# Kernel optimization log

Hardware: AMD Instinct MI355X
Metric: run time of the kernel (lower is better)

## Reference

```python
import jax, jax.numpy as jnp
import numpy as np

B, S, D_IN, D_OUT = 4, 2048, 4096, 4096
NNZ = 167772


def setup_inputs() -> dict:
    key = jax.random.key(0)
    k_x, k_w, k_b, k_v, k_r, k_c = jax.random.split(key, 6)
    x = jax.random.normal(k_x, (B, S, D_IN), dtype=jnp.float32)
    W = jax.random.normal(k_w, (D_OUT, D_IN), dtype=jnp.float32) * 0.02
    b = jax.random.normal(k_b, (D_OUT,), dtype=jnp.float32) * 0.01
    delta_vals = jax.random.normal(k_v, (NNZ,), dtype=jnp.float32) * 0.01
    delta_rows = jax.random.randint(k_r, (NNZ,), 0, D_OUT)
    delta_cols = jax.random.randint(k_c, (NNZ,), 0, D_IN)
    return {"x": x, "W": W, "b": b, "delta_vals": delta_vals,
            "delta_rows": delta_rows, "delta_cols": delta_cols}


def reference(x, W, b, delta_vals, delta_rows, delta_cols):
    # output_sparse = pruned nn.Linear(x)
    out_sparse = jnp.einsum('bsi,oi->bso', x, W) + b
    # delta_B_csr as dense [out, in] built by scatter-add (duplicate coords sum, like CSR assembly)
    delta = jnp.zeros((D_OUT, D_IN), dtype=jnp.float32).at[delta_rows, delta_cols].add(delta_vals)
    # torch.sparse.mm(delta, x2d.T).T == x2d @ delta.T, computed in fp32
    comp = jnp.einsum('bsi,oi->bso', x.astype(jnp.float32), delta).astype(x.dtype)
    return out_sparse + comp
```

## Files before the change

kernel.cpp:

```cpp
#include <hip/hip_runtime.h>
#include <hip/hip_bf16.h>
#include <stdint.h>

#define B_    4
#define S_    2048
#define DIN   4096
#define DOUT  4096
#define NNZ_  167772
#define M_    (B_*S_)

typedef __attribute__((ext_vector_type(4))) float f32x4;
typedef __attribute__((ext_vector_type(8))) short s16x8;
typedef __attribute__((ext_vector_type(8))) unsigned short u16x8;

__device__ __forceinline__ unsigned short f2bf(float f) {
    unsigned int u = __float_as_uint(f);
    u += 0x7FFFu + ((u >> 16) & 1u);
    return (unsigned short)(u >> 16);
}

__device__ __forceinline__ float bf2f(unsigned short h) {
    return __uint_as_float(((unsigned int)h) << 16);
}

__device__ __forceinline__ void gload16(const void* g, void* l) {
    __builtin_amdgcn_global_load_lds(
        (const __attribute__((address_space(1))) unsigned int*)g,
        (__attribute__((address_space(3))) unsigned int*)l,
        16, 0, 0);
}


__global__ void cvt_both_kernel(const float* __restrict__ W,
                                const float* __restrict__ x,
                                unsigned short* __restrict__ Wb,
                                unsigned short* __restrict__ xb,
                                int n8w, int n8x) {
    int i = blockIdx.x * blockDim.x + threadIdx.x;
    const float* src;
    unsigned short* dst;
    int j;
    if (i < n8w) { src = W; dst = Wb; j = i; }
    else         { src = x; dst = xb; j = i - n8w; if (j >= n8x) return; }
    const f32x4* s4 = reinterpret_cast<const f32x4*>(src);
    f32x4 a0 = s4[2*j], a1 = s4[2*j+1];
    u16x8 o;
    o[0]=f2bf(a0[0]); o[1]=f2bf(a0[1]); o[2]=f2bf(a0[2]); o[3]=f2bf(a0[3]);
    o[4]=f2bf(a1[0]); o[5]=f2bf(a1[1]); o[6]=f2bf(a1[2]); o[7]=f2bf(a1[3]);
    reinterpret_cast<u16x8*>(dst)[j] = o;
}

__global__ void scatter_bf16_kernel(const float* __restrict__ vals,
                                    const int* __restrict__ rows,
                                    const int* __restrict__ cols,
                                    unsigned short* __restrict__ Wb, int nnz) {
    int i = blockIdx.x * blockDim.x + threadIdx.x;
    if (i >= nnz) return;
    size_t cell = (size_t)rows[i] * DIN + cols[i];
    unsigned int* word = reinterpret_cast<unsigned int*>(Wb) + (cell >> 1);
    const bool hiHalf = (cell & 1) != 0;
    const float v = vals[i];
    unsigned int old = *word, assumed;
    do {
        assumed = old;
        unsigned short h = hiHalf ? (unsigned short)(assumed >> 16)
                                  : (unsigned short)(assumed & 0xFFFFu);
        unsigned short nh = f2bf(bf2f(h) + v);
        unsigned int nw = hiHalf ? ((assumed & 0x0000FFFFu) | ((unsigned int)nh << 16))
                                 : ((assumed & 0xFFFF0000u) | (unsigned int)nh);
        old = atomicCAS(word, assumed, nw);
    } while (old != assumed);
}


__global__ __launch_bounds__(512, 2) void gemm_kernel(
    const unsigned short* __restrict__ A,
    const unsigned short* __restrict__ Bw,
    const float* __restrict__ bias,
    float* __restrict__ C)
{
    constexpr int K  = DIN;
    constexpr int N  = DOUT;
    constexpr int KB = K * 2;
    extern __shared__ char smem[];

    const int tid  = threadIdx.x;
    const int wave = tid >> 6;
    const int lane = tid & 63;
    const int wr = wave >> 2;
    const int wc = wave & 3;
    const int l16 = lane & 15;
    const int kq  = lane >> 4;
    const int s7  = l16 & 7;

    const int wg  = blockIdx.x;
    const int swz = (wg & 7) * 64 + (wg >> 3);
    const int bx  = swz & 15;
    const int by  = swz >> 4;
    const int rowBase = by * 256;
    const int colBase = bx * 256;

    const int r0    = tid >> 3;
    const int gslot = (tid & 7) ^ (r0 & 7);
    const char* gA = (const char*)A  + (size_t)(rowBase + r0) * KB + gslot * 16;
    const char* gB = (const char*)Bw + (size_t)(colBase + r0) * KB + gslot * 16;
    const int wvoff = wave * 1024;

    const unsigned q0 = (unsigned)(kq ^ s7);
    const unsigned q1 = (unsigned)((4 + kq) ^ s7);
    const unsigned aBase = (unsigned)((wr * 128 + l16) * 128);
    const unsigned bBase = (unsigned)((wc * 64  + l16) * 128);
    const unsigned short* aPtr[2][2];
    const unsigned short* bPtr[2][2];
    #pragma unroll
    for (int p_ = 0; p_ < 2; ++p_) {
        aPtr[p_][0] = (const unsigned short*)(smem + p_ * 65536 + aBase + q0 * 16);
        aPtr[p_][1] = (const unsigned short*)(smem + p_ * 65536 + aBase + q1 * 16);
        bPtr[p_][0] = (const unsigned short*)(smem + p_ * 65536 + 32768 + bBase + q0 * 16);
        bPtr[p_][1] = (const unsigned short*)(smem + p_ * 65536 + 32768 + bBase + q1 * 16);
    }

    f32x4 acc[8][4];
    #pragma unroll
    for (int i = 0; i < 8; ++i)
        #pragma unroll
        for (int j = 0; j < 4; ++j) acc[i][j] = f32x4{0.f, 0.f, 0.f, 0.f};

#define STAGE_A(P, T, H) do { \
    const char* g_ = gA + (size_t)(T) * 128 + (size_t)(H) * 1048576; \
    gload16(g_,          smem + (P) * 65536 + (H) * 16384 + wvoff); \
    gload16(g_ + 524288, smem + (P) * 65536 + (H) * 16384 + 8192 + wvoff); \
} while (0)

#define STAGE_B(P, T, H) do { \
    const char* g_ = gB + (size_t)(T) * 128 + (size_t)(H) * 1048576; \
    gload16(g_,          smem + (P) * 65536 + 32768 + (H) * 16384 + wvoff); \
    gload16(g_ + 524288, smem + (P) * 65536 + 32768 + (H) * 16384 + 8192 + wvoff); \
} while (0)

#define BAR() asm volatile("s_barrier" ::: "memory")

#define TILE(P, T, SB, SA, VN) do { \
    s16x8 af0[4][2], af1[4][2], bf0[2][2], bf1[2][2]; \
     \
    _Pragma("unroll") \
    for (int m_ = 0; m_ < 4; ++m_) { \
        af0[m_][0] = *(const s16x8*)(aPtr[P][0] + m_ * 1024); \
        af0[m_][1] = *(const s16x8*)(aPtr[P][1] + m_ * 1024); } \
    _Pragma("unroll") \
    for (int n_ = 0; n_ < 2; ++n_) { \
        bf0[n_][0] = *(const s16x8*)(bPtr[P][0] + n_ * 1024); \
        bf0[n_][1] = *(const s16x8*)(bPtr[P][1] + n_ * 1024); } \
    if (SB) STAGE_B(1 - (P), (T) + 1, 0); \
    BAR(); \
    __builtin_amdgcn_s_setprio(1); \
    _Pragma("unroll") \
    for (int m_ = 0; m_ < 4; ++m_) \
      _Pragma("unroll") \
      for (int n_ = 0; n_ < 2; ++n_) { \
        acc[m_][n_] = __builtin_amdgcn_mfma_f32_16x16x32_bf16(af0[m_][0], bf0[n_][0], acc[m_][n_], 0, 0, 0); \
        acc[m_][n_] = __builtin_amdgcn_mfma_f32_16x16x32_bf16(af0[m_][1], bf0[n_][1], acc[m_][n_], 0, 0, 0); } \
    __builtin_amdgcn_s_setprio(0); \
    BAR(); \
     \
    _Pragma("unroll") \
    for (int m_ = 0; m_ < 4; ++m_) { \
        af1[m_][0] = *(const s16x8*)(aPtr[P][0] + 4096 + m_ * 1024); \
        af1[m_][1] = *(const s16x8*)(aPtr[P][1] + 4096 + m_ * 1024); } \
    if (SB) STAGE_B(1 - (P), (T) + 1, 1); \
    BAR(); \
    __builtin_amdgcn_s_setprio(1); \
    _Pragma("unroll") \
    for (int m_ = 0; m_ < 4; ++m_) \
      _Pragma("unroll") \
      for (int n_ = 0; n_ < 2; ++n_) { \
        acc[4 + m_][n_] = __builtin_amdgcn_mfma_f32_16x16x32_bf16(af1[m_][0], bf0[n_][0], acc[4 + m_][n_], 0, 0, 0); \
        acc[4 + m_][n_] = __builtin_amdgcn_mfma_f32_16x16x32_bf16(af1[m_][1], bf0[n_][1], acc[4 + m_][n_], 0, 0, 0); } \
    __builtin_amdgcn_s_setprio(0); \
    BAR(); \
     \
    _Pragma("unroll") \
    for (int n_ = 0; n_ < 2; ++n_) { \
        bf1[n_][0] = *(const s16x8*)(bPtr[P][0] + 2048 + n_ * 1024); \
        bf1[n_][1] = *(const s16x8*)(bPtr[P][1] + 2048 + n_ * 1024); } \
    if (SA) STAGE_A(P, (T) + 2, 0); \
    BAR(); \
    __builtin_amdgcn_s_setprio(1); \
    _Pragma("unroll") \
    for (int m_ = 0; m_ < 4; ++m_) \
      _Pragma("unroll") \
      for (int n_ = 0; n_ < 2; ++n_) { \
        acc[m_][2 + n_] = __builtin_amdgcn_mfma_f32_16x16x32_bf16(af0[m_][0], bf1[n_][0], acc[m_][2 + n_], 0, 0, 0); \
        acc[m_][2 + n_] = __builtin_amdgcn_mfma_f32_16x16x32_bf16(af0[m_][1], bf1[n_][1], acc[m_][2 + n_], 0, 0, 0); } \
    __builtin_amdgcn_s_setprio(0); \
    BAR(); \
     \
    if (SA) STAGE_A(P, (T) + 2, 1); \
    BAR(); \
    __builtin_amdgcn_s_setprio(1); \
    _Pragma("unroll") \
    for (int m_ = 0; m_ < 4; ++m_) \
      _Pragma("unroll") \
      for (int n_ = 0; n_ < 2; ++n_) { \
        acc[4 + m_][2 + n_] = __builtin_amdgcn_mfma_f32_16x16x32_bf16(af1[m_][0], bf1[n_][0], acc[4 + m_][2 + n_], 0, 0, 0); \
        acc[4 + m_][2 + n_] = __builtin_amdgcn_mfma_f32_16x16x32_bf16(af1[m_][1], bf1[n_][1], acc[4 + m_][2 + n_], 0, 0, 0); } \
    __builtin_amdgcn_s_setprio(0); \
     \
    if (VN) { asm volatile("s_waitcnt vmcnt(4)" ::: "memory"); } \
    else    { asm volatile("s_waitcnt vmcnt(0)" ::: "memory"); } \
    BAR(); \
} while (0)

    STAGE_A(0, 0, 0); STAGE_A(0, 0, 1);
    STAGE_B(0, 0, 0); STAGE_B(0, 0, 1);
    STAGE_A(1, 1, 0); STAGE_A(1, 1, 1);
    asm volatile("s_waitcnt vmcnt(4)" ::: "memory");
    BAR();

    #pragma unroll 1
    for (int t = 0; t < 62; t += 2) {
        TILE(0, t,     1, 1, 4);
        TILE(1, t + 1, 1, 1, 4);
    }
    TILE(0, 62, 1, 0, 0);
    TILE(1, 63, 0, 0, 0);

#undef TILE
#undef BAR
#undef STAGE_A
#undef STAGE_B

    float bv[4];
    #pragma unroll
    for (int nf = 0; nf < 4; ++nf)
        bv[nf] = bias[colBase + wc * 64 + nf * 16 + l16];

    #pragma unroll
    for (int mf = 0; mf < 8; ++mf) {
        const int rowG = rowBase + wr * 128 + mf * 16 + kq * 4;
        float* cp = C + (size_t)rowG * N + colBase + wc * 64 + l16;
        #pragma unroll
        for (int nf = 0; nf < 4; ++nf)
            #pragma unroll
            for (int j = 0; j < 4; ++j)
                cp[(size_t)j * N + nf * 16] = acc[mf][nf][j] + bv[nf];
    }
}

extern "C" void kernel_launch(void* const* d_in, const int* in_sizes, int n_in,
                              void* d_out, int out_size, void* d_ws, size_t ws_size,
                              hipStream_t stream) {
    const float* x     = (const float*)d_in[0];
    const float* W     = (const float*)d_in[1];
    const float* b     = (const float*)d_in[2];
    const float* dvals = (const float*)d_in[3];
    const int*   drows = (const int*)d_in[4];
    const int*   dcols = (const int*)d_in[5];
    float* out = (float*)d_out;

    char* ws = (char*)d_ws;
    unsigned short* Wb = (unsigned short*)ws;
    unsigned short* xb = (unsigned short*)(ws + (size_t)32 * 1024 * 1024);

    int n8w = DOUT * DIN / 8;
    int n8x = M_ * DIN / 8;
    int nblk = (n8w + n8x) / 256;
    cvt_both_kernel<<<nblk, 256, 0, stream>>>(W, x, Wb, xb, n8w, n8x);
    scatter_bf16_kernel<<<(NNZ_ + 255) / 256, 256, 0, stream>>>(dvals, drows, dcols, Wb, NNZ_);

    static bool attr_done = false;
    if (!attr_done) {
        (void)hipFuncSetAttribute(reinterpret_cast<const void*>(gemm_kernel),
                                  hipFuncAttributeMaxDynamicSharedMemorySize, 131072);
        attr_done = true;
    }
    gemm_kernel<<<dim3(512), dim3(512), 131072, stream>>>(xb, Wb, b, out);
}
```

Measured before the change: 275.6 us.

## Restructure GEMM tile pipeline to prefetch next-tile fragments and stage both operands ahead

Reorders the four MFMA quadrants in each K-tile so the first A/B fragments for the next tile are read from LDS during the current tile's last quadrants. Global-to-LDS staging of A and B for tile T+2 is moved to the end of the tile, so both operands are now double-buffered two tiles ahead. This replaces the old split where B led by one tile and A by two. The aim is to hide LDS read latency and simplify the vmcnt waits, at the cost of more live registers for fragments carried across iterations. The stricter vmcnt(0) waits and changed barrier placement could expose global-load latency or create LDS buffer hazards.

```diff
diff --git a/kernel.cpp b/kernel.cpp
--- a/kernel.cpp
+++ b/kernel.cpp
@@ -126,6 +126,8 @@
         #pragma unroll
         for (int j = 0; j < 4; ++j) acc[i][j] = f32x4{0.f, 0.f, 0.f, 0.f};
 
+    s16x8 af0[4][2], af1[4][2], bf0[2][2], bf1[2][2];
+
 #define STAGE_A(P, T, H) do { \
     const char* g_ = gA + (size_t)(T) * 128 + (size_t)(H) * 1048576; \
     gload16(g_,          smem + (P) * 65536 + (H) * 16384 + wvoff); \
@@ -140,92 +142,99 @@
 
 #define BAR() asm volatile("s_barrier" ::: "memory")
 
-#define TILE(P, T, SB, SA, VN) do { \
-    s16x8 af0[4][2], af1[4][2], bf0[2][2], bf1[2][2]; \
-     \
-    _Pragma("unroll") \
-    for (int m_ = 0; m_ < 4; ++m_) { \
-        af0[m_][0] = *(const s16x8*)(aPtr[P][0] + m_ * 1024); \
-        af0[m_][1] = *(const s16x8*)(aPtr[P][1] + m_ * 1024); } \
+#define MFMA16(D, Af, Bf) D = __builtin_amdgcn_mfma_f32_16x16x32_bf16(Af, Bf, D, 0, 0, 0)
+
+#define TILE(P, T, SS, FN) do { \
+     \
+    BAR(); \
+    __builtin_amdgcn_s_setprio(1); \
+    _Pragma("unroll") \
+    for (int m_ = 0; m_ < 4; ++m_) \
+      _Pragma("unroll") \
+      for (int n_ = 0; n_ < 2; ++n_) { \
+        MFMA16(acc[m_][n_], af0[m_][0], bf0[n_][0]); \
+        MFMA16(acc[m_][n_], af0[m_][1], bf0[n_][1]); } \
+    __builtin_amdgcn_s_setprio(0); \
     _Pragma("unroll") \
     for (int n_ = 0; n_ < 2; ++n_) { \
-        bf0[n_][0] = *(const s16x8*)(bPtr[P][0] + n_ * 1024); \
-        bf0[n_][1] = *(const s16x8*)(bPtr[P][1] + n_ * 1024); } \
-    if (SB) STAGE_B(1 - (P), (T) + 1, 0); \
-    BAR(); \
-    __builtin_amdgcn_s_setprio(1); \
-    _Pragma("unroll") \
-    for (int m_ = 0; m_ < 4; ++m_) \
-      _Pragma("unroll") \
-      for (int n_ = 0; n_ < 2; ++n_) { \
-        acc[m_][n_] = __builtin_amdgcn_mfma_f32_16x16x32_bf16(af0[m_][0], bf0[n_][0], acc[m_][n_], 0, 0, 0); \
-        acc[m_][n_] = __builtin_amdgcn_mfma_f32_16x16x32_bf16(af0[m_][1], bf0[n_][1], acc[m_][n_], 0, 0, 0); } \
-    __builtin_amdgcn_s_setprio(0); \
-    BAR(); \
-     \
+        bf1[n_][0] = *(const s16x8*)(bPtr[P][0] + 2048 + n_ * 1024); \
+        bf1[n_][1] = *(const s16x8*)(bPtr[P][1] + 2048 + n_ * 1024); } \
+     \
+    BAR(); \
+    __builtin_amdgcn_s_setprio(1); \
+    _Pragma("unroll") \
+    for (int m_ = 0; m_ < 4; ++m_) \
+      _Pragma("unroll") \
+      for (int n_ = 0; n_ < 2; ++n_) { \
+        MFMA16(acc[m_][2 + n_], af0[m_][0], bf1[n_][0]); \
+        MFMA16(acc[m_][2 + n_], af0[m_][1], bf1[n_][1]); } \
+    __builtin_amdgcn_s_setprio(0); \
     _Pragma("unroll") \
     for (int m_ = 0; m_ < 4; ++m_) { \
         af1[m_][0] = *(const s16x8*)(aPtr[P][0] + 4096 + m_ * 1024); \
         af1[m_][1] = *(const s16x8*)(aPtr[P][1] + 4096 + m_ * 1024); } \
-    if (SB) STAGE_B(1 - (P), (T) + 1, 1); \
-    BAR(); \
-    __builtin_amdgcn_s_setprio(1); \
-    _Pragma("unroll") \
-    for (int m_ = 0; m_ < 4; ++m_) \
-      _Pragma("unroll") \
-      for (int n_ = 0; n_ < 2; ++n_) { \
-        acc[4 + m_][n_] = __builtin_amdgcn_mfma_f32_16x16x32_bf16(af1[m_][0], bf0[n_][0], acc[4 + m_][n_], 0, 0, 0); \
-        acc[4 + m_][n_] = __builtin_amdgcn_mfma_f32_16x16x32_bf16(af1[m_][1], bf0[n_][1], acc[4 + m_][n_], 0, 0, 0); } \
-    __builtin_amdgcn_s_setprio(0); \
-    BAR(); \
-     \
-    _Pragma("unroll") \
-    for (int n_ = 0; n_ < 2; ++n_) { \
-        bf1[n_][0] = *(const s16x8*)(bPtr[P][0] + 2048 + n_ * 1024); \
-        bf1[n_][1] = *(const s16x8*)(bPtr[P][1] + 2048 + n_ * 1024); } \
-    if (SA) STAGE_A(P, (T) + 2, 0); \
-    BAR(); \
-    __builtin_amdgcn_s_setprio(1); \
-    _Pragma("unroll") \
-    for (int m_ = 0; m_ < 4; ++m_) \
-      _Pragma("unroll") \
-      for (int n_ = 0; n_ < 2; ++n_) { \
-        acc[m_][2 + n_] = __builtin_amdgcn_mfma_f32_16x16x32_bf16(af0[m_][0], bf1[n_][0], acc[m_][2 + n_], 0, 0, 0); \
-        acc[m_][2 + n_] = __builtin_amdgcn_mfma_f32_16x16x32_bf16(af0[m_][1], bf1[n_][1], acc[m_][2 + n_], 0, 0, 0); } \
-    __builtin_amdgcn_s_setprio(0); \
-    BAR(); \
-     \
-    if (SA) STAGE_A(P, (T) + 2, 1); \
-    BAR(); \
-    __builtin_amdgcn_s_setprio(1); \
-    _Pragma("unroll") \
-    for (int m_ = 0; m_ < 4; ++m_) \
-      _Pragma("unroll") \
-      for (int n_ = 0; n_ < 2; ++n_) { \
-        acc[4 + m_][2 + n_] = __builtin_amdgcn_mfma_f32_16x16x32_bf16(af1[m_][0], bf1[n_][0], acc[4 + m_][2 + n_], 0, 0, 0); \
-        acc[4 + m_][2 + n_] = __builtin_amdgcn_mfma_f32_16x16x32_bf16(af1[m_][1], bf1[n_][1], acc[4 + m_][2 + n_], 0, 0, 0); } \
-    __builtin_amdgcn_s_setprio(0); \
-     \
-    if (VN) { asm volatile("s_waitcnt vmcnt(4)" ::: "memory"); } \
-    else    { asm volatile("s_waitcnt vmcnt(0)" ::: "memory"); } \
-    BAR(); \
+    if (FN) { asm volatile("s_waitcnt vmcnt(0)" ::: "memory"); } \
+     \
+    BAR(); \
+    __builtin_amdgcn_s_setprio(1); \
+    _Pragma("unroll") \
+    for (int m_ = 0; m_ < 4; ++m_) \
+      _Pragma("unroll") \
+      for (int n_ = 0; n_ < 2; ++n_) { \
+        MFMA16(acc[4 + m_][2 + n_], af1[m_][0], bf1[n_][0]); \
+        MFMA16(acc[4 + m_][2 + n_], af1[m_][1], bf1[n_][1]); } \
+    __builtin_amdgcn_s_setprio(0); \
+    if (FN) { \
+      _Pragma("unroll") \
+      for (int m_ = 0; m_ < 4; ++m_) { \
+        af0[m_][0] = *(const s16x8*)(aPtr[1 - (P)][0] + m_ * 1024); \
+        af0[m_][1] = *(const s16x8*)(aPtr[1 - (P)][1] + m_ * 1024); } } \
+    if (SS) { STAGE_B(P, (T) + 2, 0); STAGE_B(P, (T) + 2, 1); } \
+     \
+    BAR(); \
+    __builtin_amdgcn_s_setprio(1); \
+    _Pragma("unroll") \
+    for (int m_ = 0; m_ < 4; ++m_) \
+      _Pragma("unroll") \
+      for (int n_ = 0; n_ < 2; ++n_) { \
+        MFMA16(acc[4 + m_][n_], af1[m_][0], bf0[n_][0]); \
+        MFMA16(acc[4 + m_][n_], af1[m_][1], bf0[n_][1]); } \
+    __builtin_amdgcn_s_setprio(0); \
+    if (FN) { \
+      _Pragma("unroll") \
+      for (int n_ = 0; n_ < 2; ++n_) { \
+        bf0[n_][0] = *(const s16x8*)(bPtr[1 - (P)][0] + n_ * 1024); \
+        bf0[n_][1] = *(const s16x8*)(bPtr[1 - (P)][1] + n_ * 1024); } } \
+    if (SS) { STAGE_A(P, (T) + 2, 0); STAGE_A(P, (T) + 2, 1); } \
 } while (0)
 
     STAGE_A(0, 0, 0); STAGE_A(0, 0, 1);
     STAGE_B(0, 0, 0); STAGE_B(0, 0, 1);
+    STAGE_B(1, 1, 0); STAGE_B(1, 1, 1);
     STAGE_A(1, 1, 0); STAGE_A(1, 1, 1);
-    asm volatile("s_waitcnt vmcnt(4)" ::: "memory");
+    asm volatile("s_waitcnt vmcnt(8)" ::: "memory");
     BAR();
+    #pragma unroll
+    for (int m_ = 0; m_ < 4; ++m_) {
+        af0[m_][0] = *(const s16x8*)(aPtr[0][0] + m_ * 1024);
+        af0[m_][1] = *(const s16x8*)(aPtr[0][1] + m_ * 1024);
+    }
+    #pragma unroll
+    for (int n_ = 0; n_ < 2; ++n_) {
+        bf0[n_][0] = *(const s16x8*)(bPtr[0][0] + n_ * 1024);
+        bf0[n_][1] = *(const s16x8*)(bPtr[0][1] + n_ * 1024);
+    }
 
     #pragma unroll 1
     for (int t = 0; t < 62; t += 2) {
-        TILE(0, t,     1, 1, 4);
-        TILE(1, t + 1, 1, 1, 4);
-    }
-    TILE(0, 62, 1, 0, 0);
-    TILE(1, 63, 0, 0, 0);
+        TILE(0, t,     1, 1);
+        TILE(1, t + 1, 1, 1);
+    }
+    TILE(0, 62, 0, 1);
+    TILE(1, 63, 0, 0);
 
 #undef TILE
+#undef MFMA16
 #undef BAR
 #undef STAGE_A
 #undef STAGE_B
```

New measurement: 267.0 us. -3.1%, faster.
